# Performance work log

Hardware: AMD Instinct MI355X
Metric: run time of the kernel (lower is better)

## Reference

```python
import jax, jax.numpy as jnp
import numpy as np

HEADS = 8
DIM_HEAD = 64
DIM = 512
SCALE = DIM ** -0.5  # NOTE: original scales by dim**-0.5, not dim_head**-0.5


def setup_inputs() -> dict:
    key = jax.random.key(0)
    k1, k2, k3 = jax.random.split(key, 3)
    b, n = 2, 4096
    x = jax.random.normal(k1, (b, n, DIM), dtype=jnp.float32)
    Wqkv = jax.random.normal(k2, (DIM, 3 * HEADS * DIM_HEAD), dtype=jnp.float32) * (DIM ** -0.5)
    Wout = jax.random.normal(k3, (HEADS * DIM_HEAD, DIM), dtype=jnp.float32) * ((HEADS * DIM_HEAD) ** -0.5)
    b_out = jnp.zeros((DIM,), dtype=jnp.float32)
    return {"x": x, "Wqkv": Wqkv, "Wout": Wout, "b_out": b_out}


def reference(x, Wqkv, Wout, b_out):
    b, n, _ = x.shape
    h, d = HEADS, DIM_HEAD
    qkv = x @ Wqkv  # [b, n, 3*h*d]
    q, k, v = jnp.split(qkv, 3, axis=-1)
    to_heads = lambda t: t.reshape(b, n, h, d).transpose(0, 2, 1, 3)  # [b,h,n,d]
    q, k, v = to_heads(q), to_heads(k), to_heads(v)
    half = n // 2
    q_s, q_t = q[:, :, :half], q[:, :, half:]
    k_t = k[:, :, half:]  # k_s is unused in the original module
    v_s, v_t = v[:, :, :half], v[:, :, half:]
    # temporal branch: q_t attends to k_t, reads v_t
    dots_t = jnp.einsum('bhid,bhjd->bhij', q_t, k_t) * SCALE
    # spatial branch: cross-term q_s attends to k_t, reads v_s
    dots_s = jnp.einsum('bhid,bhjd->bhij', q_s, k_t) * SCALE
    attn_s = jax.nn.softmax(dots_s, axis=-1)
    attn_t = jax.nn.softmax(dots_t, axis=-1)
    out_s = jnp.einsum('bhij,bhjd->bhid', attn_s, v_s)
    out_t = jnp.einsum('bhij,bhjd->bhid', attn_t, v_t)
    out = jnp.concatenate([out_s, out_t], axis=2)  # [b,h,n,d]
    out = out.transpose(0, 2, 1, 3).reshape(b, n, h * d)
    return out @ Wout + b_out
```

## Files before the change

### kernel.cpp

```cpp
#include <hip/hip_runtime.h>
#include <hip/hip_bf16.h>

typedef __bf16 bf16;
typedef _Float16 f16;
typedef __bf16 bf16x4 __attribute__((ext_vector_type(4)));
typedef __bf16 bf16x8 __attribute__((ext_vector_type(8)));
typedef _Float16 f16x2 __attribute__((ext_vector_type(2)));
typedef _Float16 f16x4 __attribute__((ext_vector_type(4)));
typedef _Float16 f16x8 __attribute__((ext_vector_type(8)));
typedef float floatx4 __attribute__((ext_vector_type(4)));

static __device__ __forceinline__ floatx4 mfma_bf16(bf16x8 a, bf16x8 b, floatx4 c) {
  return __builtin_amdgcn_mfma_f32_16x16x32_bf16(a, b, c, 0, 0, 0);
}
static __device__ __forceinline__ floatx4 mfma_f16k32(f16x8 a, f16x8 b, floatx4 c) {
  return __builtin_amdgcn_mfma_f32_16x16x32_f16(a, b, c, 0, 0, 0);
}

static __device__ __forceinline__ void async16(void* lds, const void* gp) {
  __builtin_amdgcn_global_load_lds(
      (const __attribute__((address_space(1))) void*)gp,
      (__attribute__((address_space(3))) void*)lds, 16, 0, 0);
}

static __device__ __forceinline__ bf16x8 cvt8(float4 f0, float4 f1) {
  bf16x8 r;
  r[0] = (bf16)f0.x; r[1] = (bf16)f0.y; r[2] = (bf16)f0.z; r[3] = (bf16)f0.w;
  r[4] = (bf16)f1.x; r[5] = (bf16)f1.y; r[6] = (bf16)f1.z; r[7] = (bf16)f1.w;
  return r;
}

#define HEADS 8
#define DIMH 64
#define DIM 512
#define SEQ 4096
#define HALF 2048
#define BATCH 2
#define MROWS (BATCH * SEQ)
#define ELEMS ((size_t)MROWS * DIM)
#define NPARTS 4

#define C2F (0.044194173824159216f * 1.4426950408889634f)

__global__ __launch_bounds__(256)
void prep(const float* __restrict__ X, bf16* __restrict__ Xb,
          const float* __restrict__ wqkv, bf16* __restrict__ W1t,
          const float* __restrict__ wout, bf16* __restrict__ W2t) {
  __shared__ float tile[32][33];
  const int bid = blockIdx.x, t = threadIdx.x;
  if (bid < 2048) {
    size_t i = ((size_t)bid * 256 + t) * 8;
    float4 f0 = *reinterpret_cast<const float4*>(X + i);
    float4 f1 = *reinterpret_cast<const float4*>(X + i + 4);
    *reinterpret_cast<bf16x8*>(Xb + i) = cvt8(f0, f1);
    return;
  }
  const float* src; bf16* dst; int N, id;
  if (bid < 2816) { id = bid - 2048; src = wqkv; dst = W1t; N = 1536; }
  else            { id = bid - 2816; src = wout; dst = W2t; N = 512; }
  const int nb = N / 32;
  const int n0 = (id % nb) * 32, k0 = (id / nb) * 32;
  const int r = t >> 3, c4 = (t & 7) * 4;
  float4 v = *reinterpret_cast<const float4*>(src + (size_t)(k0 + r) * N + n0 + c4);
  tile[r][c4 + 0] = v.x; tile[r][c4 + 1] = v.y;
  tile[r][c4 + 2] = v.z; tile[r][c4 + 3] = v.w;
  __syncthreads();
  bf16x4 o;
#pragma unroll
  for (int i = 0; i < 4; ++i) o[i] = (bf16)tile[c4 + i][r];
  *reinterpret_cast<bf16x4*>(dst + (size_t)(n0 + r) * DIM + k0 + c4) = o;
}

__global__ __launch_bounds__(256)
void qkv_gemm(const bf16* __restrict__ Xb, const bf16* __restrict__ Wt,
              bf16* __restrict__ Qw, bf16* __restrict__ Kw, f16* __restrict__ Vt) {
  __shared__ __align__(16) char smem_raw[36864];

  const int m0 = blockIdx.x * 128, n0 = blockIdx.y * 128;
  const int t = threadIdx.x;
  const int wave = t >> 6, lane = t & 63, quad = lane >> 4, l16 = lane & 15;
  const int wr = wave >> 1, wc = wave & 1;

  f16 (*Ts)[72] = (f16(*)[72])(smem_raw + wave * 9216);

  floatx4 acc[4][4] = {};

  auto issue = [&](int buf, int k0) {
    bf16* Asf = (bf16*)(smem_raw + buf * 16384);
    bf16* Bsf = Asf + 4096;
#pragma unroll
    for (int it = 0; it < 2; ++it) {
      int g = it * 256 + t, row = g >> 2, c8 = (g & 3) * 8;
      async16(Asf + (size_t)g * 8, Xb + (size_t)(m0 + row) * DIM + k0 + c8);
      async16(Bsf + (size_t)g * 8, Wt + (size_t)(n0 + row) * DIM + k0 + c8);
    }
  };

  issue(0, 0);
  int buf = 0;
#pragma unroll 1
  for (int k0 = 0; k0 < DIM; k0 += 32) {
    __syncthreads();
    if (k0 + 32 < DIM) issue(buf ^ 1, k0 + 32);

    const bf16* Asf = (const bf16*)(smem_raw + buf * 16384);
    const bf16* Bsf = Asf + 4096;
    bf16x8 af[4], bfr[4];
#pragma unroll
    for (int mi = 0; mi < 4; ++mi)
      af[mi] = *reinterpret_cast<const bf16x8*>(
          Asf + (size_t)(wr * 64 + mi * 16 + l16) * 32 + quad * 8);
#pragma unroll
    for (int ni = 0; ni < 4; ++ni)
      bfr[ni] = *reinterpret_cast<const bf16x8*>(
          Bsf + (size_t)(wc * 64 + ni * 16 + l16) * 32 + quad * 8);
#pragma unroll
    for (int mi = 0; mi < 4; ++mi)
#pragma unroll
      for (int ni = 0; ni < 4; ++ni)
        acc[mi][ni] = mfma_bf16(af[mi], bfr[ni], acc[mi][ni]);
    buf ^= 1;
  }

  if (n0 < 1024) {
#pragma unroll
    for (int mi = 0; mi < 4; ++mi)
#pragma unroll
      for (int ni = 0; ni < 4; ++ni)
#pragma unroll
        for (int r = 0; r < 4; ++r) {
          int row = m0 + wr * 64 + mi * 16 + quad * 4 + r;
          int col = n0 + wc * 64 + ni * 16 + l16;
          int which = col >> 9, cc = col & 511;
          int head = cc >> 6, dim = cc & 63;
          int bb = row >> 12, nn = row & 4095;
          float val = acc[mi][ni][r];
          if (which == 0) val *= C2F;
          bf16* dst = which ? Kw : Qw;
          dst[(((size_t)(bb * HEADS + head)) * SEQ + nn) * DIMH + dim] = (bf16)val;
        }
  } else {
    __syncthreads();
    int head = (n0 + wc * 64 - 1024) >> 6;
#pragma unroll
    for (int mi = 0; mi < 4; ++mi)
#pragma unroll
      for (int ni = 0; ni < 4; ++ni) {
        f16x4 pv;
#pragma unroll
        for (int r = 0; r < 4; ++r) pv[r] = (f16)acc[mi][ni][r];
        *reinterpret_cast<f16x4*>(&Ts[ni * 16 + l16][mi * 16 + quad * 4]) = pv;
      }
    int bb = m0 >> 12, nnb = (m0 + wr * 64) & 4095;
    size_t base = ((size_t)(bb * HEADS + head)) * DIMH;
#pragma unroll
    for (int it = 0; it < 8; ++it) {
      int idx = lane + it * 64;
      int d = idx >> 3, ns = (idx & 7) * 8;
      *reinterpret_cast<f16x8*>(Vt + (base + d) * SEQ + nnb + ns) =
          *reinterpret_cast<const f16x8*>(&Ts[d][ns]);
    }
  }
}

__global__ __launch_bounds__(256)
void attn_kernel(const bf16* __restrict__ Q, const bf16* __restrict__ K,
                 const f16* __restrict__ Vt, f16* __restrict__ Opart,
                 float* __restrict__ Lpart) {
  __shared__ __align__(16) char smem[16384];

  const int qt = blockIdx.x;
  const int h = blockIdx.y;
  const int bb = blockIdx.z >> 2, part = blockIdx.z & 3;
  const int t = threadIdx.x;
  const int wave = t >> 6, lane = t & 63, quad = lane >> 4, l16 = lane & 15;

  const size_t hb = ((size_t)(bb * HEADS + h)) * SEQ * DIMH;
  const int vhalf = (qt < 16) ? 0 : HALF;
  const int kstart = HALF + part * 512;
  const int vstart = vhalf + part * 512;
  const int q0 = qt * 128 + wave * 32;

  bf16x8 qa[2][2];
#pragma unroll
  for (int mt = 0; mt < 2; ++mt)
#pragma unroll
    for (int kc = 0; kc < 2; ++kc)
      qa[mt][kc] = *reinterpret_cast<const bf16x8*>(
          Q + hb + (size_t)(q0 + mt * 16 + l16) * DIMH + kc * 32 + quad * 8);

  floatx4 o_acc[2][4] = {};
  float l_acc[2] = {0.f, 0.f};

  const int r = t >> 3;
  const int rr = r & 15;
  const int kappa = (rr >> 2) * 8 + (rr & 3) + ((r & 16) ? 4 : 0);
  const int kchunk = (t & 7) ^ (r & 7);
  const bf16* kSrc = K + hb + (size_t)(kstart + kappa) * DIMH + kchunk * 8;

  const int vd = t >> 2;
  const int vchunk = (t & 3) ^ ((vd >> 1) & 3);
  const f16* vSrc = Vt + hb + (size_t)vd * SEQ + vstart + vchunk * 8;

  char* ldsK = smem + t * 16;
  char* ldsV = smem + 4096 + t * 16;

  auto issue = [&](int buf, int kc0) {
    async16(ldsK + buf * 8192, kSrc + (size_t)kc0 * DIMH);
    async16(ldsV + buf * 8192, vSrc + kc0);
  };

  const int koffA = l16 * 128 + ((quad ^ (l16 & 7)) * 16);
  const int voff = l16 * 64 + ((quad ^ ((l16 >> 1) & 3)) * 16);

  auto compute = [&](const char* Kb) {
    const char* Vb = Kb + 4096;
    bf16x8 kaA0 = *reinterpret_cast<const bf16x8*>(Kb + koffA);
    bf16x8 kaA1 = *reinterpret_cast<const bf16x8*>(Kb + (koffA ^ 64));
    bf16x8 kaB0 = *reinterpret_cast<const bf16x8*>(Kb + 2048 + koffA);
    bf16x8 kaB1 = *reinterpret_cast<const bf16x8*>(Kb + 2048 + (koffA ^ 64));

    f16x8 pbm[2];
#pragma unroll
    for (int mt = 0; mt < 2; ++mt) {
      floatx4 stA = {0.f, 0.f, 0.f, 0.f}, stB = {0.f, 0.f, 0.f, 0.f};
      stA = mfma_bf16(kaA0, qa[mt][0], stA);
      stA = mfma_bf16(kaA1, qa[mt][1], stA);
      stB = mfma_bf16(kaB0, qa[mt][0], stB);
      stB = mfma_bf16(kaB1, qa[mt][1], stB);
      float ls = l_acc[mt];
      f16x8 pb;
#pragma unroll
      for (int rr2 = 0; rr2 < 4; ++rr2) {
        float pA = __builtin_amdgcn_exp2f(stA[rr2]);
        float pB = __builtin_amdgcn_exp2f(stB[rr2]);
        ls += pA + pB;
        pb[rr2] = (f16)pA;
        pb[4 + rr2] = (f16)pB;
      }
      l_acc[mt] = ls;
      pbm[mt] = pb;
    }
#pragma unroll
    for (int dsub = 0; dsub < 4; ++dsub) {
      f16x8 va = *reinterpret_cast<const f16x8*>(Vb + voff + dsub * 1024);
      o_acc[0][dsub] = mfma_f16k32(va, pbm[0], o_acc[0][dsub]);
      o_acc[1][dsub] = mfma_f16k32(va, pbm[1], o_acc[1][dsub]);
    }
  };

  issue(0, 0);
#pragma unroll 1
  for (int kc0 = 0; kc0 < 512; kc0 += 64) {
    asm volatile("s_waitcnt vmcnt(0)" ::: "memory");
    __syncthreads();
    issue(1, kc0 + 32);
    compute(smem);
    asm volatile("s_waitcnt vmcnt(0)" ::: "memory");
    __syncthreads();
    if (kc0 + 64 < 512) issue(0, kc0 + 64);
    compute(smem + 8192);
  }

  f16* Op = Opart + (size_t)part * ELEMS;
  float* Lp = Lpart + (size_t)part * MROWS * HEADS;
#pragma unroll
  for (int mt = 0; mt < 2; ++mt) {
    float v = l_acc[mt];
    v += __shfl_xor(v, 16);
    v += __shfl_xor(v, 32);
    int n = q0 + mt * 16 + l16;
    size_t rowidx = (size_t)(bb * SEQ + n);
    if (quad == 0) Lp[rowidx * HEADS + h] = v;
    size_t rowbase = rowidx * DIM + h * DIMH;
#pragma unroll
    for (int dsub = 0; dsub < 4; ++dsub) {
      f16x4 ov;
#pragma unroll
      for (int r2 = 0; r2 < 4; ++r2) ov[r2] = (f16)o_acc[mt][dsub][r2];
      *reinterpret_cast<f16x4*>(Op + rowbase + dsub * 16 + quad * 4) = ov;
    }
  }
}

__global__ __launch_bounds__(256)
void out_gemm(const f16* __restrict__ Opart, const float* __restrict__ Lpart,
              const bf16* __restrict__ Wt, const float* __restrict__ bias,
              float* __restrict__ out) {
  __shared__ __align__(16) bf16 Asf[64 * 64];
  __shared__ __align__(16) bf16 Bsf[64 * 64];

  const int m0 = blockIdx.x * 64, n0 = blockIdx.y * 64;
  const int t = threadIdx.x;
  const int wave = t >> 6, lane = t & 63, quad = lane >> 4, l16 = lane & 15;
  const int m_off = (wave >> 1) * 32, n_off = (wave & 1) * 32;

  int srowi[2], sc8[2];
#pragma unroll
  for (int it = 0; it < 2; ++it) {
    int g = t + it * 256;
    srowi[it] = g >> 3; sc8[it] = (g & 7) * 8;
  }

  float linv[2][8];
#pragma unroll
  for (int it = 0; it < 2; ++it) {
    size_t ar = (size_t)(m0 + srowi[it]);
#pragma unroll
    for (int hh = 0; hh < 8; ++hh) {
      float s = 0.f;
#pragma unroll
      for (int p = 0; p < NPARTS; ++p)
        s += Lpart[(size_t)p * MROWS * HEADS + ar * HEADS + hh];
      linv[it][hh] = 1.0f / s;
    }
  }

  floatx4 acc[2][2] = {};

  f16x8 oreg[2][NPARTS];
  auto loadO = [&](int k0) {
#pragma unroll
    for (int it = 0; it < 2; ++it) {
      size_t abase = (size_t)(m0 + srowi[it]) * DIM + k0 + sc8[it];
#pragma unroll
      for (int p = 0; p < NPARTS; ++p)
        oreg[it][p] = *reinterpret_cast<const f16x8*>(Opart + (size_t)p * ELEMS + abase);
    }
  };

  loadO(0);
#pragma unroll 1
  for (int k0 = 0; k0 < DIM; k0 += 64) {
#pragma unroll
    for (int it = 0; it < 2; ++it) {
      int g = t + it * 256;
      async16(Bsf + (size_t)g * 8, Wt + (size_t)(n0 + srowi[it]) * DIM + k0 + sc8[it]);
      float inv = linv[it][(k0 + sc8[it]) >> 6];
      bf16x8 a;
#pragma unroll
      for (int j = 0; j < 8; ++j)
        a[j] = (bf16)(((float)oreg[it][0][j] + (float)oreg[it][1][j] +
                       (float)oreg[it][2][j] + (float)oreg[it][3][j]) * inv);
      *reinterpret_cast<bf16x8*>(Asf + (size_t)g * 8) = a;
    }
    __syncthreads();
    int nk = k0 + 64; if (nk >= DIM) nk = 0;
    loadO(nk);

#pragma unroll
    for (int kk = 0; kk < 2; ++kk) {
      bf16x8 a0 = *reinterpret_cast<const bf16x8*>(Asf + (size_t)(m_off + l16) * 64 + kk * 32 + quad * 8);
      bf16x8 a1 = *reinterpret_cast<const bf16x8*>(Asf + (size_t)(m_off + 16 + l16) * 64 + kk * 32 + quad * 8);
      bf16x8 b0 = *reinterpret_cast<const bf16x8*>(Bsf + (size_t)(n_off + l16) * 64 + kk * 32 + quad * 8);
      bf16x8 b1 = *reinterpret_cast<const bf16x8*>(Bsf + (size_t)(n_off + 16 + l16) * 64 + kk * 32 + quad * 8);
      acc[0][0] = mfma_bf16(a0, b0, acc[0][0]);
      acc[0][1] = mfma_bf16(a0, b1, acc[0][1]);
      acc[1][0] = mfma_bf16(a1, b0, acc[1][0]);
      acc[1][1] = mfma_bf16(a1, b1, acc[1][1]);
    }
    __syncthreads();
  }

#pragma unroll
  for (int mi = 0; mi < 2; ++mi)
#pragma unroll
    for (int ni = 0; ni < 2; ++ni)
#pragma unroll
      for (int r = 0; r < 4; ++r) {
        int row = m0 + m_off + mi * 16 + quad * 4 + r;
        int col = n0 + n_off + ni * 16 + l16;
        out[(size_t)row * DIM + col] = acc[mi][ni][r] + bias[col];
      }
}

extern "C" void kernel_launch(void* const* d_in, const int* in_sizes, int n_in,
                              void* d_out, int out_size, void* d_ws, size_t ws_size,
                              hipStream_t stream) {
  const float* x = (const float*)d_in[0];
  const float* wqkv = (const float*)d_in[1];
  const float* wout = (const float*)d_in[2];
  const float* bout = (const float*)d_in[3];
  float* out = (float*)d_out;

  char* ws = (char*)d_ws;
  f16* Opart = (f16*)ws;
  bf16* Xb = (bf16*)ws;
  bf16* Qw = (bf16*)(ws + ((size_t)32 << 20));
  bf16* Kw = Qw + ELEMS;
  f16* Vt = (f16*)(Kw + ELEMS);
  bf16* WtQKV = (bf16*)(Vt + ELEMS);
  bf16* WtOUT = WtQKV + (size_t)1536 * 512;
  float* Lpart = (float*)(WtOUT + (size_t)512 * 512);

  prep<<<3072, 256, 0, stream>>>(x, Xb, wqkv, WtQKV, wout, WtOUT);
  qkv_gemm<<<dim3(MROWS / 128, 1536 / 128), 256, 0, stream>>>(Xb, WtQKV, Qw, Kw, Vt);
  attn_kernel<<<dim3(SEQ / 128, HEADS, BATCH * NPARTS), 256, 0, stream>>>(Qw, Kw, Vt, Opart, Lpart);
  out_gemm<<<dim3(MROWS / 64, DIM / 64), 256, 0, stream>>>(Opart, Lpart, WtOUT, bout, out);
}
```

Baseline: 159.7 us.

## Enlarge attention blocks to 512 threads, 64-key stages, XCD-aware block mapping

The attention kernel now runs 8 waves per block covering 256 query rows and stages 64 keys per double-buffer step instead of 32. This halves the number of barriers and lets more waves reuse each K/V tile loaded into LDS. Blocks are launched on a flat grid whose index is remapped so that blocks sharing a head and key part land on the same XCD, which should improve L2 locality. MFMA sections are wrapped in s_setprio. The costs are larger shared memory per block, fewer blocks in the grid, and new swizzle arithmetic for the V layout.

```diff
diff --git a/kernel.cpp b/kernel.cpp
--- a/kernel.cpp
+++ b/kernel.cpp
@@ -163,23 +163,27 @@
   }
 }
 
-__global__ __launch_bounds__(256)
+__global__ __launch_bounds__(512)
 void attn_kernel(const bf16* __restrict__ Q, const bf16* __restrict__ K,
                  const f16* __restrict__ Vt, f16* __restrict__ Opart,
                  float* __restrict__ Lpart) {
-  __shared__ __align__(16) char smem[16384];
-
-  const int qt = blockIdx.x;
-  const int h = blockIdx.y;
-  const int bb = blockIdx.z >> 2, part = blockIdx.z & 3;
+  __shared__ __align__(16) char smem[32768];
+
+  const int bid = blockIdx.x;
+  const int xcd = bid & 7, rem = bid >> 3;
+  const int qt = rem & 15, ghi = rem >> 4;
+  const int g = (ghi << 3) | xcd;
+  const int h = g >> 3, z = g & 7;
+  const int bb = z >> 2, part = z & 3;
+
   const int t = threadIdx.x;
   const int wave = t >> 6, lane = t & 63, quad = lane >> 4, l16 = lane & 15;
 
   const size_t hb = ((size_t)(bb * HEADS + h)) * SEQ * DIMH;
-  const int vhalf = (qt < 16) ? 0 : HALF;
+  const int vhalf = (qt < 8) ? 0 : HALF;
   const int kstart = HALF + part * 512;
   const int vstart = vhalf + part * 512;
-  const int q0 = qt * 128 + wave * 32;
+  const int q0 = qt * 256 + wave * 32;
 
   bf16x8 qa[2][2];
 #pragma unroll
@@ -193,73 +197,79 @@
   float l_acc[2] = {0.f, 0.f};
 
   const int r = t >> 3;
-  const int rr = r & 15;
-  const int kappa = (rr >> 2) * 8 + (rr & 3) + ((r & 16) ? 4 : 0);
+  const int lr = r & 31, g32 = r >> 5;
+  const int rrk = lr & 15;
+  const int kappa = g32 * 32 + (rrk >> 2) * 8 + (rrk & 3) + ((lr & 16) ? 4 : 0);
   const int kchunk = (t & 7) ^ (r & 7);
   const bf16* kSrc = K + hb + (size_t)(kstart + kappa) * DIMH + kchunk * 8;
 
-  const int vd = t >> 2;
-  const int vchunk = (t & 3) ^ ((vd >> 1) & 3);
+  const int vd = t >> 3;
+  const int vchunk = (t & 7) ^ (vd & 7);
   const f16* vSrc = Vt + hb + (size_t)vd * SEQ + vstart + vchunk * 8;
 
-  char* ldsK = smem + t * 16;
-  char* ldsV = smem + 4096 + t * 16;
-
   auto issue = [&](int buf, int kc0) {
-    async16(ldsK + buf * 8192, kSrc + (size_t)kc0 * DIMH);
-    async16(ldsV + buf * 8192, vSrc + kc0);
+    async16(smem + buf * 16384 + t * 16, kSrc + (size_t)kc0 * DIMH);
+    async16(smem + buf * 16384 + 8192 + t * 16, vSrc + kc0);
   };
 
-  const int koffA = l16 * 128 + ((quad ^ (l16 & 7)) * 16);
-  const int voff = l16 * 64 + ((quad ^ ((l16 >> 1) & 3)) * 16);
+  const int ksw = (quad ^ (l16 & 7)) * 16;
+  const int koff = l16 * 128 + ksw;
 
   auto compute = [&](const char* Kb) {
-    const char* Vb = Kb + 4096;
-    bf16x8 kaA0 = *reinterpret_cast<const bf16x8*>(Kb + koffA);
-    bf16x8 kaA1 = *reinterpret_cast<const bf16x8*>(Kb + (koffA ^ 64));
-    bf16x8 kaB0 = *reinterpret_cast<const bf16x8*>(Kb + 2048 + koffA);
-    bf16x8 kaB1 = *reinterpret_cast<const bf16x8*>(Kb + 2048 + (koffA ^ 64));
-
-    f16x8 pbm[2];
-#pragma unroll
-    for (int mt = 0; mt < 2; ++mt) {
-      floatx4 stA = {0.f, 0.f, 0.f, 0.f}, stB = {0.f, 0.f, 0.f, 0.f};
-      stA = mfma_bf16(kaA0, qa[mt][0], stA);
-      stA = mfma_bf16(kaA1, qa[mt][1], stA);
-      stB = mfma_bf16(kaB0, qa[mt][0], stB);
-      stB = mfma_bf16(kaB1, qa[mt][1], stB);
-      float ls = l_acc[mt];
-      f16x8 pb;
-#pragma unroll
-      for (int rr2 = 0; rr2 < 4; ++rr2) {
-        float pA = __builtin_amdgcn_exp2f(stA[rr2]);
-        float pB = __builtin_amdgcn_exp2f(stB[rr2]);
-        ls += pA + pB;
-        pb[rr2] = (f16)pA;
-        pb[4 + rr2] = (f16)pB;
+    const char* Vb = Kb + 8192;
+    __builtin_amdgcn_s_setprio(1);
+#pragma unroll
+    for (int gk = 0; gk < 2; ++gk) {
+      const char* Kg = Kb + gk * 4096;
+      bf16x8 kaA0 = *reinterpret_cast<const bf16x8*>(Kg + koff);
+      bf16x8 kaA1 = *reinterpret_cast<const bf16x8*>(Kg + (koff ^ 64));
+      bf16x8 kaB0 = *reinterpret_cast<const bf16x8*>(Kg + 2048 + koff);
+      bf16x8 kaB1 = *reinterpret_cast<const bf16x8*>(Kg + 2048 + (koff ^ 64));
+
+      f16x8 pbm[2];
+#pragma unroll
+      for (int mt = 0; mt < 2; ++mt) {
+        floatx4 stA = {0.f, 0.f, 0.f, 0.f}, stB = {0.f, 0.f, 0.f, 0.f};
+        stA = mfma_bf16(kaA0, qa[mt][0], stA);
+        stA = mfma_bf16(kaA1, qa[mt][1], stA);
+        stB = mfma_bf16(kaB0, qa[mt][0], stB);
+        stB = mfma_bf16(kaB1, qa[mt][1], stB);
+        float ls = l_acc[mt];
+        f16x8 pb;
+#pragma unroll
+        for (int rr2 = 0; rr2 < 4; ++rr2) {
+          float pA = __builtin_amdgcn_exp2f(stA[rr2]);
+          float pB = __builtin_amdgcn_exp2f(stB[rr2]);
+          ls += pA + pB;
+          pb[rr2] = (f16)pA;
+          pb[4 + rr2] = (f16)pB;
+        }
+        l_acc[mt] = ls;
+        pbm[mt] = pb;
       }
-      l_acc[mt] = ls;
-      pbm[mt] = pb;
-    }
-#pragma unroll
-    for (int dsub = 0; dsub < 4; ++dsub) {
-      f16x8 va = *reinterpret_cast<const f16x8*>(Vb + voff + dsub * 1024);
-      o_acc[0][dsub] = mfma_f16k32(va, pbm[0], o_acc[0][dsub]);
-      o_acc[1][dsub] = mfma_f16k32(va, pbm[1], o_acc[1][dsub]);
-    }
+      const int vgo = ksw ^ (gk << 6);
+#pragma unroll
+      for (int dsub = 0; dsub < 4; ++dsub) {
+        f16x8 va = *reinterpret_cast<const f16x8*>(
+            Vb + l16 * 128 + dsub * 2048 + vgo);
+        o_acc[0][dsub] = mfma_f16k32(va, pbm[0], o_acc[0][dsub]);
+        o_acc[1][dsub] = mfma_f16k32(va, pbm[1], o_acc[1][dsub]);
+      }
+    }
+    __builtin_amdgcn_s_setprio(0);
   };
 
   issue(0, 0);
 #pragma unroll 1
-  for (int kc0 = 0; kc0 < 512; kc0 += 64) {
+  for (int kc0 = 0; kc0 < 512; kc0 += 128) {
     asm volatile("s_waitcnt vmcnt(0)" ::: "memory");
     __syncthreads();
-    issue(1, kc0 + 32);
+    issue(1, kc0 + 64);
     compute(smem);
     asm volatile("s_waitcnt vmcnt(0)" ::: "memory");
     __syncthreads();
-    if (kc0 + 64 < 512) issue(0, kc0 + 64);
-    compute(smem + 8192);
+    if (kc0 + 128 < 512) issue(0, kc0 + 128);
+    compute(smem + 16384);
   }
 
   f16* Op = Opart + (size_t)part * ELEMS;
@@ -395,6 +405,6 @@
 
   prep<<<3072, 256, 0, stream>>>(x, Xb, wqkv, WtQKV, wout, WtOUT);
   qkv_gemm<<<dim3(MROWS / 128, 1536 / 128), 256, 0, stream>>>(Xb, WtQKV, Qw, Kw, Vt);
-  attn_kernel<<<dim3(SEQ / 128, HEADS, BATCH * NPARTS), 256, 0, stream>>>(Qw, Kw, Vt, Opart, Lpart);
+  attn_kernel<<<(SEQ / 256) * HEADS * BATCH * NPARTS, 512, 0, stream>>>(Qw, Kw, Vt, Opart, Lpart);
   out_gemm<<<dim3(MROWS / 64, DIM / 64), 256, 0, stream>>>(Opart, Lpart, WtOUT, bout, out);
 }
```

Measured after the change: 161.8 us. Within noise of the previous version (+1.3%).

## Use 4-slot async K/V ring, XCD-aware block remap, and MFMA priority boost

Applied to the files above, without the earlier changes.

The attention kernel's K/V staging moves from a double buffer with full vmcnt(0) drains to a four-slot LDS ring with three loads in flight and partial waitcnts. This lets loads overlap compute across more iterations. The grid is flattened to 1D and remapped so blocks sharing a head, batch and part land on the same XCD, which should improve L2 reuse of K/V. s_setprio is raised around the compute section to favour MFMA issue. LDS per block doubles to 32 KB, which may lower occupancy.

```diff
diff --git a/kernel.cpp b/kernel.cpp
--- a/kernel.cpp
+++ b/kernel.cpp
@@ -167,11 +167,15 @@
 void attn_kernel(const bf16* __restrict__ Q, const bf16* __restrict__ K,
                  const f16* __restrict__ Vt, f16* __restrict__ Opart,
                  float* __restrict__ Lpart) {
-  __shared__ __align__(16) char smem[16384];
-
-  const int qt = blockIdx.x;
-  const int h = blockIdx.y;
-  const int bb = blockIdx.z >> 2, part = blockIdx.z & 3;
+  __shared__ __align__(16) char smem[32768];
+
+  const int bid = blockIdx.x;
+  const int xcd = bid & 7, rem = bid >> 3;
+  const int qt = rem & 31, ghi = rem >> 5;
+  const int g = ghi * 8 + xcd;
+  const int h = g >> 3, z = g & 7;
+  const int bb = z >> 2, part = z & 3;
+
   const int t = threadIdx.x;
   const int wave = t >> 6, lane = t & 63, quad = lane >> 4, l16 = lane & 15;
 
@@ -202,12 +206,9 @@
   const int vchunk = (t & 3) ^ ((vd >> 1) & 3);
   const f16* vSrc = Vt + hb + (size_t)vd * SEQ + vstart + vchunk * 8;
 
-  char* ldsK = smem + t * 16;
-  char* ldsV = smem + 4096 + t * 16;
-
-  auto issue = [&](int buf, int kc0) {
-    async16(ldsK + buf * 8192, kSrc + (size_t)kc0 * DIMH);
-    async16(ldsV + buf * 8192, vSrc + kc0);
+  auto issue = [&](int slot, int kc0) {
+    async16(smem + slot * 8192 + t * 16, kSrc + (size_t)kc0 * DIMH);
+    async16(smem + slot * 8192 + 4096 + t * 16, vSrc + kc0);
   };
 
   const int koffA = l16 * 128 + ((quad ^ (l16 & 7)) * 16);
@@ -215,6 +216,7 @@
 
   auto compute = [&](const char* Kb) {
     const char* Vb = Kb + 4096;
+    __builtin_amdgcn_s_setprio(1);
     bf16x8 kaA0 = *reinterpret_cast<const bf16x8*>(Kb + koffA);
     bf16x8 kaA1 = *reinterpret_cast<const bf16x8*>(Kb + (koffA ^ 64));
     bf16x8 kaB0 = *reinterpret_cast<const bf16x8*>(Kb + 2048 + koffA);
@@ -247,19 +249,20 @@
       o_acc[0][dsub] = mfma_f16k32(va, pbm[0], o_acc[0][dsub]);
       o_acc[1][dsub] = mfma_f16k32(va, pbm[1], o_acc[1][dsub]);
     }
+    __builtin_amdgcn_s_setprio(0);
   };
 
   issue(0, 0);
+  issue(1, 32);
+  issue(2, 64);
 #pragma unroll 1
-  for (int kc0 = 0; kc0 < 512; kc0 += 64) {
-    asm volatile("s_waitcnt vmcnt(0)" ::: "memory");
-    __syncthreads();
-    issue(1, kc0 + 32);
-    compute(smem);
-    asm volatile("s_waitcnt vmcnt(0)" ::: "memory");
-    __syncthreads();
-    if (kc0 + 64 < 512) issue(0, kc0 + 64);
-    compute(smem + 8192);
+  for (int i = 0; i < 16; ++i) {
+    if (i <= 13)      asm volatile("s_waitcnt vmcnt(4)" ::: "memory");
+    else if (i == 14) asm volatile("s_waitcnt vmcnt(2)" ::: "memory");
+    else              asm volatile("s_waitcnt vmcnt(0)" ::: "memory");
+    asm volatile("s_barrier" ::: "memory");
+    if (i <= 12) issue((i + 3) & 3, (i + 3) * 32);
+    compute(smem + (i & 3) * 8192);
   }
 
   f16* Op = Opart + (size_t)part * ELEMS;
@@ -395,6 +398,6 @@
 
   prep<<<3072, 256, 0, stream>>>(x, Xb, wqkv, WtQKV, wout, WtOUT);
   qkv_gemm<<<dim3(MROWS / 128, 1536 / 128), 256, 0, stream>>>(Xb, WtQKV, Qw, Kw, Vt);
-  attn_kernel<<<dim3(SEQ / 128, HEADS, BATCH * NPARTS), 256, 0, stream>>>(Qw, Kw, Vt, Opart, Lpart);
+  attn_kernel<<<2048, 256, 0, stream>>>(Qw, Kw, Vt, Opart, Lpart);
   out_gemm<<<dim3(MROWS / 64, DIM / 64), 256, 0, stream>>>(Opart, Lpart, WtOUT, bout, out);
 }
```

After: 156.2 us. 2.2% less time.

## Enlarge out_gemm M tile to 128 and XOR-swizzle LDS tiles

Applied to the files above, without the earlier changes.

The output projection GEMM now computes a 128x64 tile per block instead of 64x64, so each wave computes a 64x32 sub-tile. The W tile is reused across more rows, and the number of blocks that re-read the weights and redo the partial-sum combine is halved. A and B shared-memory tiles use an XOR chunk swizzle to reduce LDS bank conflicts on the fragment reads. In exchange, each thread holds more registers (4x4 f16x8 partials plus a larger accumulator array), which may lower occupancy, and the grid has half as many blocks.

```diff
diff --git a/kernel.cpp b/kernel.cpp
--- a/kernel.cpp
+++ b/kernel.cpp
@@ -287,25 +287,20 @@
 void out_gemm(const f16* __restrict__ Opart, const float* __restrict__ Lpart,
               const bf16* __restrict__ Wt, const float* __restrict__ bias,
               float* __restrict__ out) {
-  __shared__ __align__(16) bf16 Asf[64 * 64];
+  __shared__ __align__(16) bf16 Asf[128 * 64];
   __shared__ __align__(16) bf16 Bsf[64 * 64];
 
-  const int m0 = blockIdx.x * 64, n0 = blockIdx.y * 64;
+  const int m0 = blockIdx.x * 128, n0 = blockIdx.y * 64;
   const int t = threadIdx.x;
   const int wave = t >> 6, lane = t & 63, quad = lane >> 4, l16 = lane & 15;
-  const int m_off = (wave >> 1) * 32, n_off = (wave & 1) * 32;
-
-  int srowi[2], sc8[2];
-#pragma unroll
-  for (int it = 0; it < 2; ++it) {
-    int g = t + it * 256;
-    srowi[it] = g >> 3; sc8[it] = (g & 7) * 8;
-  }
-
-  float linv[2][8];
-#pragma unroll
-  for (int it = 0; it < 2; ++it) {
-    size_t ar = (size_t)(m0 + srowi[it]);
+  const int m_off = (wave >> 1) * 64, n_off = (wave & 1) * 32;
+
+  const int srow = t >> 3, schunk = t & 7;
+
+  float linv[4][8];
+#pragma unroll
+  for (int it = 0; it < 4; ++it) {
+    size_t ar = (size_t)(m0 + srow + it * 32);
 #pragma unroll
     for (int hh = 0; hh < 8; ++hh) {
       float s = 0.f;
@@ -316,13 +311,13 @@
     }
   }
 
-  floatx4 acc[2][2] = {};
-
-  f16x8 oreg[2][NPARTS];
+  floatx4 acc[4][2] = {};
+
+  f16x8 oreg[4][NPARTS];
   auto loadO = [&](int k0) {
 #pragma unroll
-    for (int it = 0; it < 2; ++it) {
-      size_t abase = (size_t)(m0 + srowi[it]) * DIM + k0 + sc8[it];
+    for (int it = 0; it < 4; ++it) {
+      size_t abase = (size_t)(m0 + srow + it * 32) * DIM + k0 + schunk * 8;
 #pragma unroll
       for (int p = 0; p < NPARTS; ++p)
         oreg[it][p] = *reinterpret_cast<const f16x8*>(Opart + (size_t)p * ELEMS + abase);
@@ -332,17 +327,25 @@
   loadO(0);
 #pragma unroll 1
   for (int k0 = 0; k0 < DIM; k0 += 64) {
+    const int head = k0 >> 6;
 #pragma unroll
     for (int it = 0; it < 2; ++it) {
-      int g = t + it * 256;
-      async16(Bsf + (size_t)g * 8, Wt + (size_t)(n0 + srowi[it]) * DIM + k0 + sc8[it]);
-      float inv = linv[it][(k0 + sc8[it]) >> 6];
+      int g = t + it * 256, brow = g >> 3;
+      int bchunk = (g & 7) ^ (brow & 7);
+      async16(Bsf + (size_t)g * 8,
+              Wt + (size_t)(n0 + brow) * DIM + k0 + bchunk * 8);
+    }
+#pragma unroll
+    for (int it = 0; it < 4; ++it) {
+      int arow = srow + it * 32;
+      float inv = linv[it][head];
       bf16x8 a;
 #pragma unroll
       for (int j = 0; j < 8; ++j)
         a[j] = (bf16)(((float)oreg[it][0][j] + (float)oreg[it][1][j] +
                        (float)oreg[it][2][j] + (float)oreg[it][3][j]) * inv);
-      *reinterpret_cast<bf16x8*>(Asf + (size_t)g * 8) = a;
+      *reinterpret_cast<bf16x8*>(
+          Asf + (size_t)arow * 64 + ((schunk ^ (arow & 7)) * 8)) = a;
     }
     __syncthreads();
     int nk = k0 + 64; if (nk >= DIM) nk = 0;
@@ -350,20 +353,30 @@
 
 #pragma unroll
     for (int kk = 0; kk < 2; ++kk) {
-      bf16x8 a0 = *reinterpret_cast<const bf16x8*>(Asf + (size_t)(m_off + l16) * 64 + kk * 32 + quad * 8);
-      bf16x8 a1 = *reinterpret_cast<const bf16x8*>(Asf + (size_t)(m_off + 16 + l16) * 64 + kk * 32 + quad * 8);
-      bf16x8 b0 = *reinterpret_cast<const bf16x8*>(Bsf + (size_t)(n_off + l16) * 64 + kk * 32 + quad * 8);
-      bf16x8 b1 = *reinterpret_cast<const bf16x8*>(Bsf + (size_t)(n_off + 16 + l16) * 64 + kk * 32 + quad * 8);
-      acc[0][0] = mfma_bf16(a0, b0, acc[0][0]);
-      acc[0][1] = mfma_bf16(a0, b1, acc[0][1]);
-      acc[1][0] = mfma_bf16(a1, b0, acc[1][0]);
-      acc[1][1] = mfma_bf16(a1, b1, acc[1][1]);
-    }
-    __syncthreads();
-  }
-
-#pragma unroll
-  for (int mi = 0; mi < 2; ++mi)
+      bf16x8 af[4], bfr[2];
+#pragma unroll
+      for (int mi = 0; mi < 4; ++mi) {
+        int row = m_off + mi * 16 + l16;
+        af[mi] = *reinterpret_cast<const bf16x8*>(
+            Asf + (size_t)row * 64 + (((kk * 4 + quad) ^ (row & 7)) * 8));
+      }
+#pragma unroll
+      for (int ni = 0; ni < 2; ++ni) {
+        int row = n_off + ni * 16 + l16;
+        bfr[ni] = *reinterpret_cast<const bf16x8*>(
+            Bsf + (size_t)row * 64 + (((kk * 4 + quad) ^ (row & 7)) * 8));
+      }
+#pragma unroll
+      for (int mi = 0; mi < 4; ++mi)
+#pragma unroll
+        for (int ni = 0; ni < 2; ++ni)
+          acc[mi][ni] = mfma_bf16(af[mi], bfr[ni], acc[mi][ni]);
+    }
+    __syncthreads();
+  }
+
+#pragma unroll
+  for (int mi = 0; mi < 4; ++mi)
 #pragma unroll
     for (int ni = 0; ni < 2; ++ni)
 #pragma unroll
@@ -396,5 +409,5 @@
   prep<<<3072, 256, 0, stream>>>(x, Xb, wqkv, WtQKV, wout, WtOUT);
   qkv_gemm<<<dim3(MROWS / 128, 1536 / 128), 256, 0, stream>>>(Xb, WtQKV, Qw, Kw, Vt);
   attn_kernel<<<dim3(SEQ / 128, HEADS, BATCH * NPARTS), 256, 0, stream>>>(Qw, Kw, Vt, Opart, Lpart);
-  out_gemm<<<dim3(MROWS / 64, DIM / 64), 256, 0, stream>>>(Opart, Lpart, WtOUT, bout, out);
-}
+  out_gemm<<<dim3(MROWS / 128, DIM / 64), 256, 0, stream>>>(Opart, Lpart, WtOUT, bout, out);
+}
```

Result: slower. 168.6 us (+5.5%).
